# Optimization experiments

Measured on AMD Instinct MI355X. Metric: run time of the kernel, lower is better.

## Reference

```python
import jax, jax.numpy as jnp
import numpy as np

N = 20000      # num_nodes
H = 150        # hidden_channels
R = 35         # num_relations
B = 5          # num_blocks  -> block dims 30x30
E = 640000     # num_edges
IB = H // B


def _xavier(key, shape):
    fan_in, fan_out = shape[-2], shape[-1]
    lim = jnp.sqrt(6.0 / (fan_in + fan_out))
    return jax.random.uniform(key, shape, jnp.float32, -lim, lim)


def setup_inputs() -> dict:
    key = jax.random.key(0)
    ks = jax.random.split(key, 10)
    edge_index = jax.random.randint(ks[0], (2, E), 0, N, dtype=jnp.int64)
    edge_type = jax.random.randint(ks[1], (E,), 0, R, dtype=jnp.int64)
    return {
        "node_emb": _xavier(ks[2], (N, H)),
        "w1": _xavier(ks[3], (R, B, IB, IB)),      # relation block-diagonal weights
        "root1": _xavier(ks[4], (H, H)),
        "b1": jnp.zeros((H,), jnp.float32),
        "w2": _xavier(ks[5], (R, B, IB, IB)),
        "root2": _xavier(ks[6], (H, H)),
        "b2": jnp.zeros((H,), jnp.float32),
        "edge_index": edge_index,
        "edge_type": edge_type,
    }


def _rgcn_layer(x, w, root, bias, src, dst, etype):
    # PyG RGCNConv with num_blocks: per-relation block-diag transform of source
    # features, mean-aggregated per (dst, relation), summed over relations,
    # plus dense root transform and bias.
    # Linearity lets us aggregate (mean) FIRST, then transform: cheaper + exact.
    seg = dst * R + etype                                   # [E] segment per (node, rel)
    xs = x[src]                                             # [E, H] gather
    sums = jax.ops.segment_sum(xs, seg, num_segments=N * R)  # [N*R, H]
    cnt = jax.ops.segment_sum(jnp.ones((src.shape[0],), x.dtype), seg,
                              num_segments=N * R)           # [N*R]
    mean = sums / jnp.maximum(cnt, 1.0)[:, None]            # zero where no edges
    a = mean.reshape(N, R, B, IB)
    agg = jnp.einsum('nrbi,rbio->nbo', a, w).reshape(N, H)  # sum over relations
    return agg + x @ root + bias


def reference(node_emb, w1, root1, b1, w2, root2, b2, edge_index, edge_type):
    src, dst = edge_index[0], edge_index[1]
    x = _rgcn_layer(node_emb, w1, root1, b1, src, dst, edge_type)
    x = jax.nn.relu(x)
    # dropout p=0.2 is a no-op in eval mode
    x = _rgcn_layer(x, w2, root2, b2, src, dst, edge_type)
    return x
```

## Files before the change

### kernel.cpp

```cpp
#include <hip/hip_runtime.h>
#include <hip/hip_fp16.h>

#define H 150
#define RNUM 35
#define BNUM 5
#define IB 30

typedef unsigned short ushort_t;
typedef unsigned int uint_t;
using bf16x8 = __attribute__((ext_vector_type(8))) short;
using f32x4  = __attribute__((ext_vector_type(4))) float;

__device__ __forceinline__ ushort_t f2bf(float x) {
    union { float f; unsigned u; } v; v.f = x;
    unsigned u = v.u;
    return (ushort_t)((u + 0x7FFF + ((u >> 16) & 1)) >> 16);
}
__device__ __forceinline__ float bfLo(uint_t u) {
    union { unsigned u; float f; } v; v.u = u << 16; return v.f;
}
__device__ __forceinline__ float bfHi(uint_t u) {
    union { unsigned u; float f; } v; v.u = u & 0xffff0000u; return v.f;
}


__global__ void k_count(const int* __restrict__ ei, const int* __restrict__ et,
                        int E_, int* __restrict__ cnt) {
    for (int e = blockIdx.x * blockDim.x + threadIdx.x; e < E_; e += gridDim.x * blockDim.x) {
        int d = ei[E_ + e];
        int r = et[e];
        atomicAdd(&cnt[d * RNUM + r], 1);
    }
}

#define SPT 2
#define SCAN_BLOCK 256
#define SCAN_SPAN (SPT * SCAN_BLOCK)

__global__ void k_scanA(const int* __restrict__ cnt, int N_,
                        int* __restrict__ blkN, int* __restrict__ blkD) {
    __shared__ int sn[SCAN_BLOCK], sd[SCAN_BLOCK];
    int t = threadIdx.x;
    int base = blockIdx.x * SCAN_SPAN + t * SPT;
    int tn = 0, td = 0;
    for (int k = 0; k < SPT; ++k) {
        int d = base + k;
        if (d < N_) {
            for (int r = 0; r < RNUM; ++r) {
                int c = cnt[d * RNUM + r];
                if (c) { tn++; td += c; }
            }
        }
    }
    sn[t] = tn; sd[t] = td;
    __syncthreads();
    if (t == 0) {
        int an = 0, ad = 0;
        for (int i = 0; i < SCAN_BLOCK; ++i) { an += sn[i]; ad += sd[i]; }
        blkN[blockIdx.x] = an; blkD[blockIdx.x] = ad;
    }
}

__global__ void k_scanB(const int* __restrict__ blkN, const int* __restrict__ blkD,
                        int* __restrict__ blkBN, int* __restrict__ blkBD, int nblk) {
    if (threadIdx.x == 0 && blockIdx.x == 0) {
        int an = 0, ad = 0;
        for (int i = 0; i < nblk; ++i) {
            blkBN[i] = an; blkBD[i] = ad;
            an += blkN[i]; ad += blkD[i];
        }
    }
}

__global__ void k_scanC(const int* __restrict__ cnt, int N_,
                        const int* __restrict__ blkBN, const int* __restrict__ blkBD,
                        int* __restrict__ dstbase, int* __restrict__ segoff,
                        int* __restrict__ segidx, int* __restrict__ relhist2) {
    __shared__ int sn[SCAN_BLOCK], sd[SCAN_BLOCK];
    __shared__ int lhist[RNUM];
    int t = threadIdx.x;
    for (int i = t; i < RNUM; i += SCAN_BLOCK) lhist[i] = 0;
    int base = blockIdx.x * SCAN_SPAN + t * SPT;
    int tn = 0, td = 0;
    for (int k = 0; k < SPT; ++k) {
        int d = base + k;
        if (d < N_) {
            for (int r = 0; r < RNUM; ++r) {
                int c = cnt[d * RNUM + r];
                if (c) { tn++; td += c; }
            }
        }
    }
    sn[t] = tn; sd[t] = td;
    __syncthreads();
    if (t == 0) {
        int an = blkBN[blockIdx.x], ad = blkBD[blockIdx.x];
        for (int i = 0; i < SCAN_BLOCK; ++i) {
            int a = sn[i], b = sd[i];
            sn[i] = an; sd[i] = ad;
            an += a; ad += b;
        }
    }
    __syncthreads();
    int sb = sn[t], eb = sd[t];
    for (int k = 0; k < SPT; ++k) {
        int d = base + k;
        if (d < N_) {
            dstbase[d] = sb;
            for (int r = 0; r < RNUM; ++r) {
                int cell = d * RNUM + r;
                int c = cnt[cell];
                segoff[cell] = eb;
                if (c) { segidx[cell] = sb; sb++; eb += c; atomicAdd(&lhist[r], 1); }
            }
            if (d == N_ - 1) dstbase[N_] = sb;
        }
    }
    __syncthreads();
    for (int i = t; i < RNUM; i += SCAN_BLOCK)
        if (lhist[i]) atomicAdd(&relhist2[i], lhist[i]);
}

__global__ void k_relbase(const int* __restrict__ relhist2, int* __restrict__ relbase2,
                          int* __restrict__ tprefix) {
    if (threadIdx.x == 0 && blockIdx.x == 0) {
        int a = 0, tp = 0;
        for (int r = 0; r < RNUM; ++r) {
            relbase2[r] = a; tprefix[r] = tp;
            a += relhist2[r];
            tp += (relhist2[r] + 15) >> 4;
        }
        relbase2[RNUM] = a; tprefix[RNUM] = tp;
    }
}

__global__ void k_scatter2(const int* __restrict__ ei, const int* __restrict__ et,
                           int E_, int* __restrict__ segoff, int* __restrict__ ssrc2) {
    int e = blockIdx.x * blockDim.x + threadIdx.x;
    if (e >= E_) return;
    int r = et[e];
    int d = ei[E_ + e];
    int pos = atomicAdd(&segoff[d * RNUM + r], 1);
    ssrc2[pos] = ei[e];
}

__global__ void k_relassign(const int* __restrict__ cnt, const int* __restrict__ segoff,
                            const int* __restrict__ segidx, int Ncells,
                            const int* __restrict__ relbase2, int* __restrict__ relfill2,
                            int4* __restrict__ rec) {
    __shared__ int lh[RNUM];
    __shared__ int lbase[RNUM];
    for (int i = threadIdx.x; i < RNUM; i += blockDim.x) lh[i] = 0;
    __syncthreads();
    const int stride = gridDim.x * blockDim.x;
    for (int cell = blockIdx.x * blockDim.x + threadIdx.x; cell < Ncells; cell += stride)
        if (cnt[cell]) atomicAdd(&lh[cell % RNUM], 1);
    __syncthreads();
    for (int i = threadIdx.x; i < RNUM; i += blockDim.x) {
        int c = lh[i];
        lbase[i] = relbase2[i] + (c ? atomicAdd(&relfill2[i], c) : 0);
        lh[i] = 0;
    }
    __syncthreads();
    for (int cell = blockIdx.x * blockDim.x + threadIdx.x; cell < Ncells; cell += stride) {
        int c = cnt[cell];
        if (c) {
            int r = cell % RNUM;
            int pos = lbase[r] + atomicAdd(&lh[r], 1);
            rec[pos] = make_int4(segidx[cell], segoff[cell] - c, c, 0);
        }
    }
}

__global__ void k_prepw(const float* __restrict__ w1, const float* __restrict__ w2,
                        ushort_t* __restrict__ wb1, ushort_t* __restrict__ wb2) {
    const int tot = RNUM * BNUM * 2 * 16 * 32;
    int idx = blockIdx.x * blockDim.x + threadIdx.x;
    if (idx >= 2 * tot) return;
    const float* w = (idx < tot) ? w1 : w2;
    ushort_t* wb = (idx < tot) ? wb1 : wb2;
    int q = (idx < tot) ? idx : idx - tot;
    int kj = q & 7;
    int kg = (q >> 3) & 3;
    int cl = (q >> 5) & 15;
    int nh = (q >> 9) & 1;
    int rb = q >> 10;
    int k = kg * 8 + kj;
    int col = nh * 16 + cl;
    ushort_t v = 0;
    if (k < IB && col < IB) v = f2bf(w[(rb * IB + k) * IB + col]);
    wb[q] = v;
}

__global__ void k_convA(const float* __restrict__ x, ushort_t* __restrict__ xbf, int N_) {
    int i = blockIdx.x * blockDim.x + threadIdx.x;
    if (i >= N_ * 160) return;
    int n = i / 160, c = i - n * 160;
    xbf[i] = (c < H) ? f2bf(x[n * H + c]) : 0;
}

__global__ void k_convB(const float* __restrict__ r1, const float* __restrict__ r2,
                        ushort_t* __restrict__ B1, ushort_t* __restrict__ B2) {
    int i = blockIdx.x * blockDim.x + threadIdx.x;
    if (i >= 2 * 160 * 160) return;
    const float* src = (i < 160 * 160) ? r1 : r2;
    ushort_t* dst = (i < 160 * 160) ? B1 : B2;
    int k = (i < 160 * 160) ? i : i - 160 * 160;
    int row = k / 160, col = k - row * 160;
    dst[k] = (row < H && col < H) ? f2bf(src[row * H + col]) : 0;
}

__global__ __launch_bounds__(256) void k_rootmm(const ushort_t* __restrict__ Abf,
                                                const ushort_t* __restrict__ Bbf,
                                                const float* __restrict__ bias,
                                                float* __restrict__ Cout, int N_) {
    int nt = blockIdx.y;
    int wv = threadIdx.x >> 6, l = threadIdx.x & 63;
    int lr = l & 15, lk = l >> 4;
    bf16x8 bfr[5];
    #pragma unroll
    for (int ks = 0; ks < 5; ++ks) {
        #pragma unroll
        for (int j = 0; j < 8; ++j)
            bfr[ks][j] = (short)Bbf[(ks * 32 + lk * 8 + j) * 160 + nt * 16 + lr];
    }
    int mtiles = N_ / 16;
    int col = nt * 16 + lr;
    float bv = (col < H) ? bias[col] : 0.f;
    for (int mt = blockIdx.x * 4 + wv; mt < mtiles; mt += gridDim.x * 4) {
        f32x4 acc = {0.f, 0.f, 0.f, 0.f};
        const ushort_t* arow = Abf + (size_t)(mt * 16 + lr) * 160 + lk * 8;
        #pragma unroll
        for (int ks = 0; ks < 5; ++ks) {
            bf16x8 af = *reinterpret_cast<const bf16x8*>(arow + ks * 32);
            acc = __builtin_amdgcn_mfma_f32_16x16x32_bf16(af, bfr[ks], acc, 0, 0, 0);
        }
        if (col < H) {
            #pragma unroll
            for (int reg = 0; reg < 4; ++reg)
                Cout[(size_t)(mt * 16 + lk * 4 + reg) * H + col] = acc[reg] + bv;
        }
    }
}


#define ASTRIDE 168

__global__ __launch_bounds__(256, 4)
void k_seg(const int4* __restrict__ rec, const int* __restrict__ relbase2,
           const int* __restrict__ tprefix,
           const int* __restrict__ ssrc2, const ushort_t* __restrict__ wbf,
           const ushort_t* __restrict__ xbf, __half* __restrict__ tseg,
           const int* __restrict__ rowLoP, const int* __restrict__ rowHiP) {
    __shared__ ushort_t Abuf[4][16 * ASTRIDE];
    __shared__ int relb[RNUM + 1], tpre[RNUM + 1];
    int t = threadIdx.x, wv = t >> 6, l = t & 63;
    int lr = l & 15, kg = l >> 4;
    if (t < RNUM + 1) { relb[t] = relbase2[t]; tpre[t] = tprefix[t]; }

    {
        uint_t* az = reinterpret_cast<uint_t*>(&Abuf[wv][0]);
        for (int i = l; i < 16 * ASTRIDE / 2; i += 64) az[i] = 0;
    }
    __syncthreads();
    int rowLo = rowLoP[0], rowHi = rowHiP[0];
    int ntile_tot = tpre[RNUM];

    int i0 = 2 * l;
    int uA = ((i0 / 30) * 32 + (i0 % 30)) >> 1;
    int i1 = 128 + 2 * l;
    int uB = ((i1 / 30) * 32 + (i1 % 30)) >> 1;

    for (int ti = blockIdx.x * 4 + wv; ti < ntile_tot; ti += gridDim.x * 4) {
        int r_lo = 0, r_hi = RNUM;
        while (r_hi - r_lo > 1) {
            int m = (r_lo + r_hi) >> 1;
            if (tpre[m] <= ti) r_lo = m; else r_hi = m;
        }
        int r = r_lo;
        int base = relb[r];
        int nseg = relb[r + 1] - base;
        int sbeg = (ti - tpre[r]) << 4;

        bf16x8 bfr[BNUM][2];
        #pragma unroll
        for (int b = 0; b < BNUM; ++b)
            #pragma unroll
            for (int nh = 0; nh < 2; ++nh)
                bfr[b][nh] = *reinterpret_cast<const bf16x8*>(
                    wbf + ((size_t)((r * BNUM + b) * 2 + nh) * 512) + lr * 32 + kg * 8);

        int4 myrec = make_int4(0x7fffffff, 0, 1, 0);
        if (l < 16 && sbeg + l < nseg) myrec = rec[base + sbeg + l];

        uint_t* Au = reinterpret_cast<uint_t*>(&Abuf[wv][0]);
        for (int s = 0; s < 16; ++s) {
            int row = __builtin_amdgcn_readfirstlane(__shfl(myrec.x, s));
            if (row < rowLo || row >= rowHi) continue;
            int eo = __builtin_amdgcn_readfirstlane(__shfl(myrec.y, s));
            int c  = __builtin_amdgcn_readfirstlane(__shfl(myrec.z, s));
            int src0 = ssrc2[eo];
            const uint_t* rowU = reinterpret_cast<const uint_t*>(xbf + (size_t)src0 * 160);
            uint_t u0 = rowU[l];
            uint_t u1 = 0;
            if (l < 11) u1 = rowU[64 + l];
            if (c == 1) {
                Au[s * 84 + uA] = u0;
                if (l < 11) Au[s * 84 + uB] = u1;
            } else {
                float a0 = bfLo(u0), a1 = bfHi(u0);
                float a2 = bfLo(u1), a3 = bfHi(u1);
                for (int k = 1; k < c; ++k) {
                    int src = ssrc2[eo + k];
                    const uint_t* rU = reinterpret_cast<const uint_t*>(
                        xbf + (size_t)src * 160);
                    uint_t v0 = rU[l];
                    a0 += bfLo(v0); a1 += bfHi(v0);
                    if (l < 11) {
                        uint_t v1 = rU[64 + l];
                        a2 += bfLo(v1); a3 += bfHi(v1);
                    }
                }
                float inv = 1.0f / (float)c;
                Au[s * 84 + uA] = (uint_t)f2bf(a0 * inv) | ((uint_t)f2bf(a1 * inv) << 16);
                if (l < 11)
                    Au[s * 84 + uB] = (uint_t)f2bf(a2 * inv) | ((uint_t)f2bf(a3 * inv) << 16);
            }
        }

        int rg[4]; bool rok[4];
        #pragma unroll
        for (int q = 0; q < 4; ++q) {
            rg[q] = __shfl(myrec.x, kg * 4 + q);
            rok[q] = (rg[q] >= rowLo) && (rg[q] < rowHi);
        }

        #pragma unroll
        for (int b = 0; b < BNUM; ++b) {
            bf16x8 af = *reinterpret_cast<const bf16x8*>(
                &Abuf[wv][lr * ASTRIDE + b * 32 + kg * 8]);
            f32x4 z = {0.f, 0.f, 0.f, 0.f};
            f32x4 acc0 = __builtin_amdgcn_mfma_f32_16x16x32_bf16(af, bfr[b][0], z, 0, 0, 0);
            f32x4 acc1 = __builtin_amdgcn_mfma_f32_16x16x32_bf16(af, bfr[b][1], z, 0, 0, 0);
            #pragma unroll
            for (int q = 0; q < 4; ++q) {
                if (rok[q]) {
                    __half* orow = tseg + (size_t)(rg[q] - rowLo) * H + b * IB;
                    orow[lr] = __float2half(acc0[q]);
                    if (lr < 14) orow[16 + lr] = __float2half(acc1[q]);
                }
            }
        }
    }
}


__global__ __launch_bounds__(256)
void k_aggadd(const __half* __restrict__ tseg, const int* __restrict__ dstbase,
              const float* __restrict__ rootsrc, float* __restrict__ fout,
              ushort_t* __restrict__ Abf, int relu, int s0, int s1) {
    int t = threadIdx.x, wv = t >> 6, l = t & 63;
    int segBase = dstbase[s0];
    for (int d = s0 + blockIdx.x * 4 + wv; d < s1; d += gridDim.x * 4) {
        int a = dstbase[d], bnd = dstbase[d + 1];
        const float* brow = rootsrc + (size_t)d * H;
        float2 acc0 = *reinterpret_cast<const float2*>(brow + 2 * l);
        float2 acc1 = make_float2(0.f, 0.f);
        if (l < 11) acc1 = *reinterpret_cast<const float2*>(brow + 128 + 2 * l);
        for (int s = a; s < bnd; ++s) {
            const __half2* trow = reinterpret_cast<const __half2*>(
                tseg + (size_t)(s - segBase) * H);
            float2 v = __half22float2(trow[l]);
            acc0.x += v.x; acc0.y += v.y;
            if (l < 11) {
                float2 v1 = __half22float2(trow[64 + l]);
                acc1.x += v1.x; acc1.y += v1.y;
            }
        }
        if (relu) {
            acc0.x = fmaxf(acc0.x, 0.f); acc0.y = fmaxf(acc0.y, 0.f);
            acc1.x = fmaxf(acc1.x, 0.f); acc1.y = fmaxf(acc1.y, 0.f);
        }
        if (fout) {
            float* frow = fout + (size_t)d * H;
            *reinterpret_cast<float2*>(frow + 2 * l) = acc0;
            if (l < 11) *reinterpret_cast<float2*>(frow + 128 + 2 * l) = acc1;
        }
        if (Abf) {
            ushort_t* arow = Abf + (size_t)d * 160;
            uint_t p0 = (uint_t)f2bf(acc0.x) | ((uint_t)f2bf(acc0.y) << 16);
            *reinterpret_cast<uint_t*>(arow + 2 * l) = p0;
            if (l < 11) {
                uint_t p1 = (uint_t)f2bf(acc1.x) | ((uint_t)f2bf(acc1.y) << 16);
                *reinterpret_cast<uint_t*>(arow + 128 + 2 * l) = p1;
            }
            if (l < 5) *reinterpret_cast<uint_t*>(arow + 150 + 2 * l) = 0;
        }
    }
}

extern "C" void kernel_launch(void* const* d_in, const int* in_sizes, int n_in,
                              void* d_out, int out_size, void* d_ws, size_t ws_size,
                              hipStream_t stream) {
    const float* node_emb = (const float*)d_in[0];
    const float* w1 = (const float*)d_in[1];
    const float* root1 = (const float*)d_in[2];
    const float* b1 = (const float*)d_in[3];
    const float* w2 = (const float*)d_in[4];
    const float* root2 = (const float*)d_in[5];
    const float* b2 = (const float*)d_in[6];
    const int* edge_index = (const int*)d_in[7];
    const int* edge_type = (const int*)d_in[8];
    int N_ = in_sizes[0] / H;
    int E_ = in_sizes[8];
    float* out = (float*)d_out;

    const int Ncells = N_ * RNUM;
    const int wbtot = RNUM * BNUM * 2 * 16 * 32;

    int* ws = (int*)d_ws;
    size_t off = 0;
    int* cnt      = ws + off; off += Ncells;
    int* relhist2 = ws + off; off += 64;
    int* relfill2 = ws + off; off += 64;
    size_t zero_units = off;
    int* relbase2 = ws + off; off += 64;
    int* tprefix  = ws + off; off += 64;
    int* blkN     = ws + off; off += 64;
    int* blkD     = ws + off; off += 64;
    int* blkBN    = ws + off; off += 64;
    int* blkBD    = ws + off; off += 64;
    int* dstbase  = ws + off; off += N_ + 2;
    int* segoff   = ws + off; off += Ncells;
    int* segidx   = ws + off; off += Ncells;
    int* ssrc2    = ws + off; off += E_;
    off = (off + 3) & ~(size_t)3;
    int4* rec     = (int4*)(ws + off); off += (size_t)4 * Ncells;
    ushort_t* wbf1 = (ushort_t*)(ws + off); off += wbtot / 2;
    ushort_t* wbf2 = (ushort_t*)(ws + off); off += wbtot / 2;
    ushort_t* Bbf1 = (ushort_t*)(ws + off); off += 12800;
    ushort_t* Bbf2 = (ushort_t*)(ws + off); off += 12800;
    ushort_t* xbf  = (ushort_t*)(ws + off); off += (size_t)N_ * 160 / 2;
    ushort_t* Abf  = (ushort_t*)(ws + off); off += (size_t)N_ * 160 / 2;
    float* rootbuf = (float*)(ws + off); off += (size_t)N_ * H;
    __half* tseg  = (__half*)(ws + off);
    size_t tsegOffB = off * 4;

    size_t availB = (ws_size > tsegOffB) ? (ws_size - tsegOffB) : 0;
    long long dps_ll = (long long)(availB / ((size_t)RNUM * H * 2));
    int dps = (dps_ll > N_) ? N_ : (int)dps_ll;
    if (dps < 1) dps = 1;
    int nstripe = (N_ + dps - 1) / dps;

    hipMemsetAsync(cnt, 0, zero_units * 4, stream);

    k_count<<<512, 256, 0, stream>>>(edge_index, edge_type, E_, cnt);
    int nscan = (N_ + SCAN_SPAN - 1) / SCAN_SPAN;
    k_scanA<<<nscan, SCAN_BLOCK, 0, stream>>>(cnt, N_, blkN, blkD);
    k_scanB<<<1, 64, 0, stream>>>(blkN, blkD, blkBN, blkBD, nscan);
    k_scanC<<<nscan, SCAN_BLOCK, 0, stream>>>(cnt, N_, blkBN, blkBD, dstbase, segoff,
                                              segidx, relhist2);
    k_relbase<<<1, 64, 0, stream>>>(relhist2, relbase2, tprefix);
    k_scatter2<<<(E_ + 255) / 256, 256, 0, stream>>>(edge_index, edge_type, E_, segoff, ssrc2);
    k_relassign<<<64, 256, 0, stream>>>(cnt, segoff, segidx, Ncells, relbase2, relfill2, rec);
    k_prepw<<<(2 * wbtot + 255) / 256, 256, 0, stream>>>(w1, w2, wbf1, wbf2);
    k_convB<<<(2 * 160 * 160 + 255) / 256, 256, 0, stream>>>(root1, root2, Bbf1, Bbf2);
    k_convA<<<(N_ * 160 + 255) / 256, 256, 0, stream>>>(node_emb, xbf, N_);

    const int SEG_GRID = 1792;

    k_rootmm<<<dim3(40, 10), 256, 0, stream>>>(xbf, Bbf1, b1, rootbuf, N_);
    for (int st = 0; st < nstripe; ++st) {
        int s0 = st * dps;
        int s1 = s0 + dps; if (s1 > N_) s1 = N_;
        k_seg<<<SEG_GRID, 256, 0, stream>>>(rec, relbase2, tprefix, ssrc2, wbf1, xbf, tseg,
                                            dstbase + s0, dstbase + s1);
        k_aggadd<<<1280, 256, 0, stream>>>(tseg, dstbase, rootbuf, (float*)nullptr, Abf,
                                           1, s0, s1);
    }

    k_rootmm<<<dim3(40, 10), 256, 0, stream>>>(Abf, Bbf2, b2, out, N_);
    for (int st = 0; st < nstripe; ++st) {
        int s0 = st * dps;
        int s1 = s0 + dps; if (s1 > N_) s1 = N_;
        k_seg<<<SEG_GRID, 256, 0, stream>>>(rec, relbase2, tprefix, ssrc2, wbf2, Abf, tseg,
                                            dstbase + s0, dstbase + s1);
        k_aggadd<<<1280, 256, 0, stream>>>(tseg, dstbase, out, out, (ushort_t*)nullptr,
                                           0, s0, s1);
    }
}
```

Baseline: 448.2 us.

## Fuse CSR scan kernels into a single-pass scan and merge prep conversions

```diff
diff --git a/kernel.cpp b/kernel.cpp
--- a/kernel.cpp
+++ b/kernel.cpp
@@ -5,6 +5,7 @@
 #define RNUM 35
 #define BNUM 5
 #define IB 30
+#define CSTR 36
 
 typedef unsigned short ushort_t;
 typedef unsigned int uint_t;
@@ -29,108 +30,81 @@
     for (int e = blockIdx.x * blockDim.x + threadIdx.x; e < E_; e += gridDim.x * blockDim.x) {
         int d = ei[E_ + e];
         int r = et[e];
-        atomicAdd(&cnt[d * RNUM + r], 1);
-    }
-}
-
-#define SPT 2
-#define SCAN_BLOCK 256
-#define SCAN_SPAN (SPT * SCAN_BLOCK)
-
-__global__ void k_scanA(const int* __restrict__ cnt, int N_,
-                        int* __restrict__ blkN, int* __restrict__ blkD) {
-    __shared__ int sn[SCAN_BLOCK], sd[SCAN_BLOCK];
+        atomicAdd(&cnt[d * CSTR + r], 1);
+    }
+}
+
+__global__ __launch_bounds__(256)
+void k_scan1(const int* __restrict__ cnt, int N_,
+             int* __restrict__ gcnt,
+             int* __restrict__ relfill2,
+             int* __restrict__ dstbase, int* __restrict__ dstN,
+             int* __restrict__ segoff, int4* __restrict__ rec) {
+    __shared__ int sn[256], sd[256];
+    __shared__ int lh[RNUM], lbase[RNUM];
+    __shared__ int bases[2];
     int t = threadIdx.x;
-    int base = blockIdx.x * SCAN_SPAN + t * SPT;
+    int d = blockIdx.x * 256 + t;
+    for (int i = t; i < RNUM; i += 256) lh[i] = 0;
+    __syncthreads();
+
+    int4 buf[9];
     int tn = 0, td = 0;
-    for (int k = 0; k < SPT; ++k) {
-        int d = base + k;
-        if (d < N_) {
-            for (int r = 0; r < RNUM; ++r) {
-                int c = cnt[d * RNUM + r];
-                if (c) { tn++; td += c; }
-            }
+    if (d < N_) {
+        const int4* cp = reinterpret_cast<const int4*>(cnt + (size_t)d * CSTR);
+        #pragma unroll
+        for (int q = 0; q < 9; ++q) buf[q] = cp[q];
+        const int* cc = reinterpret_cast<const int*>(buf);
+        #pragma unroll
+        for (int r = 0; r < RNUM; ++r) {
+            int c = cc[r];
+            if (c) { tn++; td += c; atomicAdd(&lh[r], 1); }
         }
     }
     sn[t] = tn; sd[t] = td;
     __syncthreads();
+    for (int i = t; i < RNUM; i += 256) {
+        int c = lh[i];
+        lbase[i] = c ? atomicAdd(&relfill2[i], c) : 0;
+        lh[i] = 0;
+    }
     if (t == 0) {
         int an = 0, ad = 0;
-        for (int i = 0; i < SCAN_BLOCK; ++i) { an += sn[i]; ad += sd[i]; }
-        blkN[blockIdx.x] = an; blkD[blockIdx.x] = ad;
-    }
-}
-
-__global__ void k_scanB(const int* __restrict__ blkN, const int* __restrict__ blkD,
-                        int* __restrict__ blkBN, int* __restrict__ blkBD, int nblk) {
-    if (threadIdx.x == 0 && blockIdx.x == 0) {
-        int an = 0, ad = 0;
-        for (int i = 0; i < nblk; ++i) {
-            blkBN[i] = an; blkBD[i] = ad;
-            an += blkN[i]; ad += blkD[i];
-        }
-    }
-}
-
-__global__ void k_scanC(const int* __restrict__ cnt, int N_,
-                        const int* __restrict__ blkBN, const int* __restrict__ blkBD,
-                        int* __restrict__ dstbase, int* __restrict__ segoff,
-                        int* __restrict__ segidx, int* __restrict__ relhist2) {
-    __shared__ int sn[SCAN_BLOCK], sd[SCAN_BLOCK];
-    __shared__ int lhist[RNUM];
-    int t = threadIdx.x;
-    for (int i = t; i < RNUM; i += SCAN_BLOCK) lhist[i] = 0;
-    int base = blockIdx.x * SCAN_SPAN + t * SPT;
-    int tn = 0, td = 0;
-    for (int k = 0; k < SPT; ++k) {
-        int d = base + k;
-        if (d < N_) {
-            for (int r = 0; r < RNUM; ++r) {
-                int c = cnt[d * RNUM + r];
-                if (c) { tn++; td += c; }
-            }
-        }
-    }
-    sn[t] = tn; sd[t] = td;
-    __syncthreads();
-    if (t == 0) {
-        int an = blkBN[blockIdx.x], ad = blkBD[blockIdx.x];
-        for (int i = 0; i < SCAN_BLOCK; ++i) {
+        for (int i = 0; i < 256; ++i) {
             int a = sn[i], b = sd[i];
             sn[i] = an; sd[i] = ad;
             an += a; ad += b;
         }
+        bases[0] = atomicAdd(&gcnt[0], an);
+        bases[1] = atomicAdd(&gcnt[1], ad);
     }
     __syncthreads();
-    int sb = sn[t], eb = sd[t];
-    for (int k = 0; k < SPT; ++k) {
-        int d = base + k;
-        if (d < N_) {
-            dstbase[d] = sb;
-            for (int r = 0; r < RNUM; ++r) {
-                int cell = d * RNUM + r;
-                int c = cnt[cell];
-                segoff[cell] = eb;
-                if (c) { segidx[cell] = sb; sb++; eb += c; atomicAdd(&lhist[r], 1); }
+    if (d < N_) {
+        int sb = bases[0] + sn[t];
+        int eb = bases[1] + sd[t];
+        dstbase[d] = sb;
+        dstN[d] = tn;
+        const int* cc = reinterpret_cast<const int*>(buf);
+        for (int r = 0; r < RNUM; ++r) {
+            int c = cc[r];
+            segoff[(size_t)d * CSTR + r] = eb;
+            if (c) {
+                int rank = atomicAdd(&lh[r], 1);
+                rec[(size_t)r * N_ + lbase[r] + rank] = make_int4(sb, eb, c, 0);
+                sb++; eb += c;
             }
-            if (d == N_ - 1) dstbase[N_] = sb;
-        }
-    }
-    __syncthreads();
-    for (int i = t; i < RNUM; i += SCAN_BLOCK)
-        if (lhist[i]) atomicAdd(&relhist2[i], lhist[i]);
-}
-
-__global__ void k_relbase(const int* __restrict__ relhist2, int* __restrict__ relbase2,
-                          int* __restrict__ tprefix) {
+        }
+    }
+}
+
+__global__ void k_relbase2(const int* __restrict__ relfill2, int* __restrict__ tprefix) {
     if (threadIdx.x == 0 && blockIdx.x == 0) {
-        int a = 0, tp = 0;
+        int tp = 0;
         for (int r = 0; r < RNUM; ++r) {
-            relbase2[r] = a; tprefix[r] = tp;
-            a += relhist2[r];
-            tp += (relhist2[r] + 15) >> 4;
-        }
-        relbase2[RNUM] = a; tprefix[RNUM] = tp;
+            tprefix[r] = tp;
+            tp += (relfill2[r] + 15) >> 4;
+        }
+        tprefix[RNUM] = tp;
     }
 }
 
@@ -140,74 +114,47 @@
     if (e >= E_) return;
     int r = et[e];
     int d = ei[E_ + e];
-    int pos = atomicAdd(&segoff[d * RNUM + r], 1);
+    int pos = atomicAdd(&segoff[(size_t)d * CSTR + r], 1);
     ssrc2[pos] = ei[e];
 }
 
-__global__ void k_relassign(const int* __restrict__ cnt, const int* __restrict__ segoff,
-                            const int* __restrict__ segidx, int Ncells,
-                            const int* __restrict__ relbase2, int* __restrict__ relfill2,
-                            int4* __restrict__ rec) {
-    __shared__ int lh[RNUM];
-    __shared__ int lbase[RNUM];
-    for (int i = threadIdx.x; i < RNUM; i += blockDim.x) lh[i] = 0;
-    __syncthreads();
-    const int stride = gridDim.x * blockDim.x;
-    for (int cell = blockIdx.x * blockDim.x + threadIdx.x; cell < Ncells; cell += stride)
-        if (cnt[cell]) atomicAdd(&lh[cell % RNUM], 1);
-    __syncthreads();
-    for (int i = threadIdx.x; i < RNUM; i += blockDim.x) {
-        int c = lh[i];
-        lbase[i] = relbase2[i] + (c ? atomicAdd(&relfill2[i], c) : 0);
-        lh[i] = 0;
-    }
-    __syncthreads();
-    for (int cell = blockIdx.x * blockDim.x + threadIdx.x; cell < Ncells; cell += stride) {
-        int c = cnt[cell];
-        if (c) {
-            int r = cell % RNUM;
-            int pos = lbase[r] + atomicAdd(&lh[r], 1);
-            rec[pos] = make_int4(segidx[cell], segoff[cell] - c, c, 0);
-        }
-    }
-}
-
-__global__ void k_prepw(const float* __restrict__ w1, const float* __restrict__ w2,
-                        ushort_t* __restrict__ wb1, ushort_t* __restrict__ wb2) {
+__global__ void k_prep(const float* __restrict__ w1, const float* __restrict__ w2,
+                       ushort_t* __restrict__ wb1, ushort_t* __restrict__ wb2,
+                       const float* __restrict__ r1, const float* __restrict__ r2,
+                       ushort_t* __restrict__ B1, ushort_t* __restrict__ B2,
+                       const float* __restrict__ x, ushort_t* __restrict__ xbf, int N_) {
     const int tot = RNUM * BNUM * 2 * 16 * 32;
-    int idx = blockIdx.x * blockDim.x + threadIdx.x;
-    if (idx >= 2 * tot) return;
-    const float* w = (idx < tot) ? w1 : w2;
-    ushort_t* wb = (idx < tot) ? wb1 : wb2;
-    int q = (idx < tot) ? idx : idx - tot;
-    int kj = q & 7;
-    int kg = (q >> 3) & 3;
-    int cl = (q >> 5) & 15;
-    int nh = (q >> 9) & 1;
-    int rb = q >> 10;
-    int k = kg * 8 + kj;
-    int col = nh * 16 + cl;
-    ushort_t v = 0;
-    if (k < IB && col < IB) v = f2bf(w[(rb * IB + k) * IB + col]);
-    wb[q] = v;
-}
-
-__global__ void k_convA(const float* __restrict__ x, ushort_t* __restrict__ xbf, int N_) {
-    int i = blockIdx.x * blockDim.x + threadIdx.x;
-    if (i >= N_ * 160) return;
-    int n = i / 160, c = i - n * 160;
-    xbf[i] = (c < H) ? f2bf(x[n * H + c]) : 0;
-}
-
-__global__ void k_convB(const float* __restrict__ r1, const float* __restrict__ r2,
-                        ushort_t* __restrict__ B1, ushort_t* __restrict__ B2) {
-    int i = blockIdx.x * blockDim.x + threadIdx.x;
-    if (i >= 2 * 160 * 160) return;
-    const float* src = (i < 160 * 160) ? r1 : r2;
-    ushort_t* dst = (i < 160 * 160) ? B1 : B2;
-    int k = (i < 160 * 160) ? i : i - 160 * 160;
-    int row = k / 160, col = k - row * 160;
-    dst[k] = (row < H && col < H) ? f2bf(src[row * H + col]) : 0;
+    const int t2 = 2 * tot;
+    const int t3 = t2 + 2 * 160 * 160;
+    const long long t4 = (long long)t3 + (long long)N_ * 160;
+    long long i = (long long)blockIdx.x * blockDim.x + threadIdx.x;
+    if (i < t2) {
+        int idx = (int)i;
+        const float* w = (idx < tot) ? w1 : w2;
+        ushort_t* wb = (idx < tot) ? wb1 : wb2;
+        int q = (idx < tot) ? idx : idx - tot;
+        int kj = q & 7;
+        int kg = (q >> 3) & 3;
+        int cl = (q >> 5) & 15;
+        int nh = (q >> 9) & 1;
+        int rb = q >> 10;
+        int k = kg * 8 + kj;
+        int col = nh * 16 + cl;
+        ushort_t v = 0;
+        if (k < IB && col < IB) v = f2bf(w[(rb * IB + k) * IB + col]);
+        wb[q] = v;
+    } else if (i < t3) {
+        int k = (int)(i - t2);
+        const float* src = (k < 160 * 160) ? r1 : r2;
+        ushort_t* dst = (k < 160 * 160) ? B1 : B2;
+        if (k >= 160 * 160) k -= 160 * 160;
+        int row = k / 160, col = k - row * 160;
+        dst[k] = (row < H && col < H) ? f2bf(src[row * H + col]) : 0;
+    } else if (i < t4) {
+        long long k = i - t3;
+        int n = (int)(k / 160), c = (int)(k - (long long)n * 160);
+        xbf[k] = (c < H) ? f2bf(x[(size_t)n * H + c]) : 0;
+    }
 }
 
 __global__ __launch_bounds__(256) void k_rootmm(const ushort_t* __restrict__ Abf,
@@ -247,23 +194,23 @@
 #define ASTRIDE 168
 
 __global__ __launch_bounds__(256, 4)
-void k_seg(const int4* __restrict__ rec, const int* __restrict__ relbase2,
+void k_seg(const int4* __restrict__ rec, const int* __restrict__ relcnt,
            const int* __restrict__ tprefix,
            const int* __restrict__ ssrc2, const ushort_t* __restrict__ wbf,
            const ushort_t* __restrict__ xbf, __half* __restrict__ tseg,
-           const int* __restrict__ rowLoP, const int* __restrict__ rowHiP) {
+           int rmLo, int rmHi, int N_, int* __restrict__ ctr) {
     __shared__ ushort_t Abuf[4][16 * ASTRIDE];
-    __shared__ int relb[RNUM + 1], tpre[RNUM + 1];
+    __shared__ int rcnt[RNUM], tpre[RNUM + 1];
     int t = threadIdx.x, wv = t >> 6, l = t & 63;
     int lr = l & 15, kg = l >> 4;
-    if (t < RNUM + 1) { relb[t] = relbase2[t]; tpre[t] = tprefix[t]; }
+    if (t < RNUM + 1) tpre[t] = tprefix[t];
+    if (t < RNUM) rcnt[t] = relcnt[t];
 
     {
         uint_t* az = reinterpret_cast<uint_t*>(&Abuf[wv][0]);
         for (int i = l; i < 16 * ASTRIDE / 2; i += 64) az[i] = 0;
     }
     __syncthreads();
-    int rowLo = rowLoP[0], rowHi = rowHiP[0];
     int ntile_tot = tpre[RNUM];
 
     int i0 = 2 * l;
@@ -271,16 +218,20 @@
     int i1 = 128 + 2 * l;
     int uB = ((i1 / 30) * 32 + (i1 % 30)) >> 1;
 
-    for (int ti = blockIdx.x * 4 + wv; ti < ntile_tot; ti += gridDim.x * 4) {
+    while (true) {
+        int tkt = 0;
+        if (l == 0) tkt = atomicAdd(ctr, 1);
+        tkt = __shfl(tkt, 0);
+        if (tkt >= ntile_tot) break;
+
         int r_lo = 0, r_hi = RNUM;
         while (r_hi - r_lo > 1) {
             int m = (r_lo + r_hi) >> 1;
-            if (tpre[m] <= ti) r_lo = m; else r_hi = m;
+            if (tpre[m] <= tkt) r_lo = m; else r_hi = m;
         }
         int r = r_lo;
-        int base = relb[r];
-        int nseg = relb[r + 1] - base;
-        int sbeg = (ti - tpre[r]) << 4;
+        int nseg = rcnt[r];
+        int sbeg = (tkt - tpre[r]) << 4;
 
         bf16x8 bfr[BNUM][2];
         #pragma unroll
@@ -291,12 +242,12 @@
                     wbf + ((size_t)((r * BNUM + b) * 2 + nh) * 512) + lr * 32 + kg * 8);
 
         int4 myrec = make_int4(0x7fffffff, 0, 1, 0);
-        if (l < 16 && sbeg + l < nseg) myrec = rec[base + sbeg + l];
+        if (l < 16 && sbeg + l < nseg) myrec = rec[(size_t)r * N_ + sbeg + l];
 
         uint_t* Au = reinterpret_cast<uint_t*>(&Abuf[wv][0]);
         for (int s = 0; s < 16; ++s) {
             int row = __builtin_amdgcn_readfirstlane(__shfl(myrec.x, s));
-            if (row < rowLo || row >= rowHi) continue;
+            if (row < rmLo || row >= rmHi) continue;
             int eo = __builtin_amdgcn_readfirstlane(__shfl(myrec.y, s));
             int c  = __builtin_amdgcn_readfirstlane(__shfl(myrec.z, s));
             int src0 = ssrc2[eo];
@@ -332,7 +283,7 @@
         #pragma unroll
         for (int q = 0; q < 4; ++q) {
             rg[q] = __shfl(myrec.x, kg * 4 + q);
-            rok[q] = (rg[q] >= rowLo) && (rg[q] < rowHi);
+            rok[q] = (rg[q] >= rmLo) && (rg[q] < rmHi);
         }
 
         #pragma unroll
@@ -345,7 +296,7 @@
             #pragma unroll
             for (int q = 0; q < 4; ++q) {
                 if (rok[q]) {
-                    __half* orow = tseg + (size_t)(rg[q] - rowLo) * H + b * IB;
+                    __half* orow = tseg + (size_t)(rg[q] - rmLo) * H + b * IB;
                     orow[lr] = __float2half(acc0[q]);
                     if (lr < 14) orow[16 + lr] = __float2half(acc1[q]);
                 }
@@ -357,19 +308,22 @@
 
 __global__ __launch_bounds__(256)
 void k_aggadd(const __half* __restrict__ tseg, const int* __restrict__ dstbase,
-              const float* __restrict__ rootsrc, float* __restrict__ fout,
-              ushort_t* __restrict__ Abf, int relu, int s0, int s1) {
+              const int* __restrict__ dstN, float* __restrict__ buf,
+              ushort_t* __restrict__ Abf, int relu, int finalize,
+              int rmLo, int rmHi, int N_, int* __restrict__ ctr) {
     int t = threadIdx.x, wv = t >> 6, l = t & 63;
-    int segBase = dstbase[s0];
-    for (int d = s0 + blockIdx.x * 4 + wv; d < s1; d += gridDim.x * 4) {
-        int a = dstbase[d], bnd = dstbase[d + 1];
-        const float* brow = rootsrc + (size_t)d * H;
+    if (blockIdx.x == 0 && t == 0) *ctr = 0;
+    for (int d = blockIdx.x * 4 + wv; d < N_; d += gridDim.x * 4) {
+        int a = dstbase[d];
+        int bnd = a + dstN[d];
+        float* brow = buf + (size_t)d * H;
         float2 acc0 = *reinterpret_cast<const float2*>(brow + 2 * l);
         float2 acc1 = make_float2(0.f, 0.f);
         if (l < 11) acc1 = *reinterpret_cast<const float2*>(brow + 128 + 2 * l);
         for (int s = a; s < bnd; ++s) {
+            if (s < rmLo || s >= rmHi) continue;
             const __half2* trow = reinterpret_cast<const __half2*>(
-                tseg + (size_t)(s - segBase) * H);
+                tseg + (size_t)(s - rmLo) * H);
             float2 v = __half22float2(trow[l]);
             acc0.x += v.x; acc0.y += v.y;
             if (l < 11) {
@@ -377,16 +331,13 @@
                 acc1.x += v1.x; acc1.y += v1.y;
             }
         }
-        if (relu) {
+        if (finalize && relu) {
             acc0.x = fmaxf(acc0.x, 0.f); acc0.y = fmaxf(acc0.y, 0.f);
             acc1.x = fmaxf(acc1.x, 0.f); acc1.y = fmaxf(acc1.y, 0.f);
         }
-        if (fout) {
-            float* frow = fout + (size_t)d * H;
-            *reinterpret_cast<float2*>(frow + 2 * l) = acc0;
-            if (l < 11) *reinterpret_cast<float2*>(frow + 128 + 2 * l) = acc1;
-        }
-        if (Abf) {
+        *reinterpret_cast<float2*>(brow + 2 * l) = acc0;
+        if (l < 11) *reinterpret_cast<float2*>(brow + 128 + 2 * l) = acc1;
+        if (finalize && Abf) {
             ushort_t* arow = Abf + (size_t)d * 160;
             uint_t p0 = (uint_t)f2bf(acc0.x) | ((uint_t)f2bf(acc0.y) << 16);
             *reinterpret_cast<uint_t*>(arow + 2 * l) = p0;
@@ -415,27 +366,22 @@
     int E_ = in_sizes[8];
     float* out = (float*)d_out;
 
-    const int Ncells = N_ * RNUM;
     const int wbtot = RNUM * BNUM * 2 * 16 * 32;
 
     int* ws = (int*)d_ws;
     size_t off = 0;
-    int* cnt      = ws + off; off += Ncells;
-    int* relhist2 = ws + off; off += 64;
+    int* cnt      = ws + off; off += (size_t)N_ * CSTR;
     int* relfill2 = ws + off; off += 64;
+    int* gcnt     = ws + off; off += 16;
+    int* ctr      = ws + off; off += 16;
     size_t zero_units = off;
-    int* relbase2 = ws + off; off += 64;
     int* tprefix  = ws + off; off += 64;
-    int* blkN     = ws + off; off += 64;
-    int* blkD     = ws + off; off += 64;
-    int* blkBN    = ws + off; off += 64;
-    int* blkBD    = ws + off; off += 64;
     int* dstbase  = ws + off; off += N_ + 2;
-    int* segoff   = ws + off; off += Ncells;
-    int* segidx   = ws + off; off += Ncells;
+    int* dstN     = ws + off; off += N_ + 2;
+    int* segoff   = ws + off; off += (size_t)N_ * CSTR;
     int* ssrc2    = ws + off; off += E_;
     off = (off + 3) & ~(size_t)3;
-    int4* rec     = (int4*)(ws + off); off += (size_t)4 * Ncells;
+    int4* rec     = (int4*)(ws + off); off += (size_t)4 * RNUM * N_;
     ushort_t* wbf1 = (ushort_t*)(ws + off); off += wbtot / 2;
     ushort_t* wbf2 = (ushort_t*)(ws + off); off += wbtot / 2;
     ushort_t* Bbf1 = (ushort_t*)(ws + off); off += 12800;
@@ -447,45 +393,46 @@
     size_t tsegOffB = off * 4;
 
     size_t availB = (ws_size > tsegOffB) ? (ws_size - tsegOffB) : 0;
-    long long dps_ll = (long long)(availB / ((size_t)RNUM * H * 2));
-    int dps = (dps_ll > N_) ? N_ : (int)dps_ll;
-    if (dps < 1) dps = 1;
-    int nstripe = (N_ + dps - 1) / dps;
+    long long maxRows = (long long)((E_ < N_ * RNUM) ? E_ : N_ * RNUM);
+    long long rps_ll = (long long)(availB / ((size_t)H * 2));
+    long long rps = (rps_ll > maxRows) ? maxRows : rps_ll;
+    if (rps < 1) rps = 1;
+    int nstripe = (int)((maxRows + rps - 1) / rps);
 
     hipMemsetAsync(cnt, 0, zero_units * 4, stream);
 
     k_count<<<512, 256, 0, stream>>>(edge_index, edge_type, E_, cnt);
-    int nscan = (N_ + SCAN_SPAN - 1) / SCAN_SPAN;
-    k_scanA<<<nscan, SCAN_BLOCK, 0, stream>>>(cnt, N_, blkN, blkD);
-    k_scanB<<<1, 64, 0, stream>>>(blkN, blkD, blkBN, blkBD, nscan);
-    k_scanC<<<nscan, SCAN_BLOCK, 0, stream>>>(cnt, N_, blkBN, blkBD, dstbase, segoff,
-                                              segidx, relhist2);
-    k_relbase<<<1, 64, 0, stream>>>(relhist2, relbase2, tprefix);
+    k_scan1<<<(N_ + 255) / 256, 256, 0, stream>>>(cnt, N_, gcnt, relfill2,
+                                                  dstbase, dstN, segoff, rec);
+    k_relbase2<<<1, 64, 0, stream>>>(relfill2, tprefix);
     k_scatter2<<<(E_ + 255) / 256, 256, 0, stream>>>(edge_index, edge_type, E_, segoff, ssrc2);
-    k_relassign<<<64, 256, 0, stream>>>(cnt, segoff, segidx, Ncells, relbase2, relfill2, rec);
-    k_prepw<<<(2 * wbtot + 255) / 256, 256, 0, stream>>>(w1, w2, wbf1, wbf2);
-    k_convB<<<(2 * 160 * 160 + 255) / 256, 256, 0, stream>>>(root1, root2, Bbf1, Bbf2);
-    k_convA<<<(N_ * 160 + 255) / 256, 256, 0, stream>>>(node_emb, xbf, N_);
+    long long preptot = 2LL * wbtot + 2 * 160 * 160 + (long long)N_ * 160;
+    k_prep<<<(int)((preptot + 255) / 256), 256, 0, stream>>>(
+        w1, w2, wbf1, wbf2, root1, root2, Bbf1, Bbf2, node_emb, xbf, N_);
 
     const int SEG_GRID = 1792;
 
     k_rootmm<<<dim3(40, 10), 256, 0, stream>>>(xbf, Bbf1, b1, rootbuf, N_);
     for (int st = 0; st < nstripe; ++st) {
-        int s0 = st * dps;
-        int s1 = s0 + dps; if (s1 > N_) s1 = N_;
-        k_seg<<<SEG_GRID, 256, 0, stream>>>(rec, relbase2, tprefix, ssrc2, wbf1, xbf, tseg,
-                                            dstbase + s0, dstbase + s1);
-        k_aggadd<<<1280, 256, 0, stream>>>(tseg, dstbase, rootbuf, (float*)nullptr, Abf,
-                                           1, s0, s1);
+        int rmLo = (int)((long long)st * rps);
+        long long hi = (long long)rmLo + rps;
+        int rmHi = (hi > maxRows) ? (int)maxRows : (int)hi;
+        int fin = (st == nstripe - 1);
+        k_seg<<<SEG_GRID, 256, 0, stream>>>(rec, relfill2, tprefix, ssrc2, wbf1, xbf,
+                                            tseg, rmLo, rmHi, N_, ctr);
+        k_aggadd<<<1280, 256, 0, stream>>>(tseg, dstbase, dstN, rootbuf, Abf, 1, fin,
+                                           rmLo, rmHi, N_, ctr);
     }
 
     k_rootmm<<<dim3(40, 10), 256, 0, stream>>>(Abf, Bbf2, b2, out, N_);
     for (int st = 0; st < nstripe; ++st) {
-        int s0 = st * dps;
-        int s1 = s0 + dps; if (s1 > N_) s1 = N_;
-        k_seg<<<SEG_GRID, 256, 0, stream>>>(rec, relbase2, tprefix, ssrc2, wbf2, Abf, tseg,
-                                            dstbase + s0, dstbase + s1);
-        k_aggadd<<<1280, 256, 0, stream>>>(tseg, dstbase, out, out, (ushort_t*)nullptr,
-                                           0, s0, s1);
-    }
-}
+        int rmLo = (int)((long long)st * rps);
+        long long hi = (long long)rmLo + rps;
+        int rmHi = (hi > maxRows) ? (int)maxRows : (int)hi;
+        int fin = (st == nstripe - 1);
+        k_seg<<<SEG_GRID, 256, 0, stream>>>(rec, relfill2, tprefix, ssrc2, wbf2, Abf,
+                                            tseg, rmLo, rmHi, N_, ctr);
+        k_aggadd<<<1280, 256, 0, stream>>>(tseg, dstbase, dstN, out, (ushort_t*)nullptr,
+                                           0, fin, rmLo, rmHi, N_, ctr);
+    }
+}
```

Result: slower. 1.010 ms (+125.3%).
